# Optimization experiments

Measured on AMD Instinct MI355X. Metric: run time of the kernel, lower is better.

Reference implementation:

```python
import jax, jax.numpy as jnp
import numpy as np

BN_EPS = 1e-5


def _bn(x, gamma, beta, mean, var):
    # inference-form BatchNorm2d over channel dim of NCHW
    inv = gamma / jnp.sqrt(var + BN_EPS)
    return x * inv[None, :, None, None] + (beta - mean * inv)[None, :, None, None]


def _conv(x, w, pad):
    return jax.lax.conv_general_dilated(
        x, w, window_strides=(1, 1), padding=[(pad, pad), (pad, pad)],
        dimension_numbers=("NCHW", "OIHW", "NCHW"))


def setup_inputs() -> dict:
    key = jax.random.key(0)
    ks = jax.random.split(key, 5)
    B, Cin, H, W = 16, 256, 80, 80
    N, Dg, E, Co = 80, 512, 128, 256  # classes, guide dim, embed ch, out ch
    M = 8  # heads
    init = lambda k, shape, fan: jax.random.normal(k, shape, jnp.float32) / np.float32(np.sqrt(fan))
    return {
        "x": jax.random.normal(ks[0], (B, Cin, H, W), jnp.float32),
        "guide": jax.random.normal(ks[1], (B, N, Dg), jnp.float32),
        "embed_w": init(ks[2], (E, Cin, 1, 1), Cin),
        "embed_bn_gamma": jnp.ones((E,), jnp.float32),
        "embed_bn_beta": jnp.zeros((E,), jnp.float32),
        "embed_bn_mean": jnp.zeros((E,), jnp.float32),
        "embed_bn_var": jnp.ones((E,), jnp.float32),
        "guide_w": init(ks[3], (E, Dg), Dg),
        "guide_b": jnp.zeros((E,), jnp.float32),
        "attn_bias": jnp.zeros((M,), jnp.float32),
        "proj_w": init(ks[4], (Co, Cin, 3, 3), Cin * 9),
        "proj_bn_gamma": jnp.ones((Co,), jnp.float32),
        "proj_bn_beta": jnp.zeros((Co,), jnp.float32),
        "proj_bn_mean": jnp.zeros((Co,), jnp.float32),
        "proj_bn_var": jnp.ones((Co,), jnp.float32),
    }


def reference(x, guide, embed_w, embed_bn_gamma, embed_bn_beta, embed_bn_mean,
              embed_bn_var, guide_w, guide_b, attn_bias, proj_w,
              proj_bn_gamma, proj_bn_beta, proj_bn_mean, proj_bn_var):
    B, _, H, W = x.shape
    N = guide.shape[1]
    M = attn_bias.shape[0]
    E = embed_w.shape[0]
    C = E // M  # attn head channels
    # guide projection: [B,N,Dg] -> [B,N,M,C]
    g = (guide @ guide_w.T + guide_b).reshape(B, N, M, C)
    # embed conv (1x1, BN, no act): [B,E,H,W] -> [B,M,C,H,W]
    e = _bn(_conv(x, embed_w, 0), embed_bn_gamma, embed_bn_beta,
            embed_bn_mean, embed_bn_var).reshape(B, M, C, H, W)
    # cross-modal scores, max over classes
    attn = jnp.einsum("bmchw,bnmc->bmhwn", e, g)  # [B,M,H,W,N]
    attn = jnp.max(attn, axis=-1) / float(np.sqrt(C))
    attn = jax.nn.sigmoid(attn + attn_bias[None, :, None, None])  # [B,M,H,W]
    # project conv (3x3, BN, SiLU) and gate per head
    p = jax.nn.silu(_bn(_conv(x, proj_w, 1), proj_bn_gamma, proj_bn_beta,
                        proj_bn_mean, proj_bn_var))
    Co = p.shape[1]
    p = p.reshape(B, M, Co // M, H, W) * attn[:, :, None]
    return p.reshape(B, Co, H, W)
```

## Files before the change

### kernel.cpp

```cpp
#include <hip/hip_runtime.h>
#include <stdint.h>

#define BB 16
#define CIN 256
#define HH 80
#define WW 80
#define HWP (HH*WW)
#define NN 80
#define DG 512
#define EE 128
#define MM 8
#define CC 16
#define CO 256

typedef unsigned short bfu;
typedef _Float16 f16;
typedef _Float16 f16x8 __attribute__((ext_vector_type(8)));
typedef float f32x4 __attribute__((ext_vector_type(4)));

__device__ __forceinline__ float b2f(bfu u) {
    union { uint32_t i; float f; } v; v.i = ((uint32_t)u) << 16; return v.f;
}
__device__ __forceinline__ bfu f2b(float f) {
    union { float f; uint32_t i; } v; v.f = f;
    uint32_t i = v.i;
    return (bfu)((i + 0x7FFFu + ((i >> 16) & 1u)) >> 16);
}
__device__ __forceinline__ float ld(const void* p, size_t i, int f32) {
    if (f32) return ((const float*)p)[i];
    return b2f(((const bfu*)p)[i]);
}
__device__ __forceinline__ int dtf32(const void* dtp) {
    return (((const uint32_t*)dtp)[0] == 0x3F800000u) ? 1 : 0;
}

__device__ __forceinline__ void gld_lds16(const f16* g, f16* l) {
    __builtin_amdgcn_global_load_lds(
        (const __attribute__((address_space(1))) void*)g,
        (__attribute__((address_space(3))) void*)l,
        16, 0, 0);
}

__global__ __launch_bounds__(128) void k_guide(
    const void* __restrict__ guide, const void* __restrict__ guide_w,
    const void* __restrict__ guide_b,
    const void* __restrict__ bng, const void* __restrict__ bnb,
    const void* __restrict__ bnm, const void* __restrict__ bnv,
    float* __restrict__ gs, float* __restrict__ gb)
{
    __shared__ float gld[DG];
    __shared__ float gwL[64][129];
    __shared__ float sh[EE];
    const int f32 = dtf32(bnv);
    const int t = threadIdx.x;
    const int bn = blockIdx.x;
    size_t gbase = (size_t)bn * DG;
    for (int d = t; d < DG; d += 128) gld[d] = ld(guide, gbase + d, f32);
    const int dd = t & 63, eh = t >> 6;
    float acc = 0.f;
    for (int d0 = 0; d0 < DG; d0 += 64) {
        __syncthreads();
        #pragma unroll
        for (int k = 0; k < 64; ++k)
            gwL[dd][eh + 2 * k] = ld(guide_w, (size_t)(eh + 2 * k) * DG + d0 + dd, f32);
        __syncthreads();
        #pragma unroll 8
        for (int d2 = 0; d2 < 64; ++d2)
            acc += gld[d0 + d2] * gwL[d2][t];
    }
    acc += ld(guide_b, t, f32);
    float inv   = ld(bng, t, f32) * rsqrtf(ld(bnv, t, f32) + 1e-5f);
    float shift = ld(bnb, t, f32) - ld(bnm, t, f32) * inv;
    gs[(size_t)bn * EE + t] = acc * inv;
    sh[t] = acc * shift;
    __syncthreads();
    if ((t & 15) == 0) {
        float s = 0.f;
        #pragma unroll
        for (int c = 0; c < 16; ++c) s += sh[t + c];
        gb[bn * MM + (t >> 4)] = s;
    }
}

__global__ __launch_bounds__(256) void k_guidemm(
    const f16* __restrict__ gwH, const f16* __restrict__ guideH,
    const void* __restrict__ guide_b,
    const void* __restrict__ bng, const void* __restrict__ bnb,
    const void* __restrict__ bnm, const void* __restrict__ bnv,
    float* __restrict__ gs, float* __restrict__ gb)
{
    const int f32 = dtf32(bnv);
    const int bn0 = blockIdx.x * 16;
    const int t = threadIdx.x;
    const int w = t >> 6, l = t & 63;
    const int lane15 = l & 15, kg = l >> 4;
    const int e0 = w * 32;

    f32x4 acc0 = {0.f, 0.f, 0.f, 0.f};
    f32x4 acc1 = {0.f, 0.f, 0.f, 0.f};

    const f16* ga  = guideH + (size_t)(bn0 + lane15) * DG + kg * 8;
    const f16* wa0 = gwH + (size_t)(e0 + lane15) * DG + kg * 8;
    const f16* wa1 = gwH + (size_t)(e0 + 16 + lane15) * DG + kg * 8;
    #pragma unroll 4
    for (int d0 = 0; d0 < DG; d0 += 32) {
        f16x8 B  = *(const f16x8*)(ga + d0);
        f16x8 A0 = *(const f16x8*)(wa0 + d0);
        f16x8 A1 = *(const f16x8*)(wa1 + d0);
        acc0 = __builtin_amdgcn_mfma_f32_16x16x32_f16(A0, B, acc0, 0, 0, 0);
        acc1 = __builtin_amdgcn_mfma_f32_16x16x32_f16(A1, B, acc1, 0, 0, 0);
    }
    const int bn = bn0 + lane15;
    float gbp0 = 0.f, gbp1 = 0.f;
    #pragma unroll
    for (int rg = 0; rg < 4; ++rg) {
        {
            int e = e0 + kg * 4 + rg;
            float g = acc0[rg] + ld(guide_b, e, f32);
            float inv   = ld(bng, e, f32) * rsqrtf(ld(bnv, e, f32) + 1e-5f);
            float shift = ld(bnb, e, f32) - ld(bnm, e, f32) * inv;
            gs[(size_t)bn * EE + e] = g * inv;
            gbp0 += g * shift;
        }
        {
            int e = e0 + 16 + kg * 4 + rg;
            float g = acc1[rg] + ld(guide_b, e, f32);
            float inv   = ld(bng, e, f32) * rsqrtf(ld(bnv, e, f32) + 1e-5f);
            float shift = ld(bnb, e, f32) - ld(bnm, e, f32) * inv;
            gs[(size_t)bn * EE + e] = g * inv;
            gbp1 += g * shift;
        }
    }
    gbp0 += __shfl_xor(gbp0, 16);
    gbp0 += __shfl_xor(gbp0, 32);
    gbp1 += __shfl_xor(gbp1, 16);
    gbp1 += __shfl_xor(gbp1, 32);
    if (kg == 0) {
        gb[bn * MM + w * 2 + 0] = gbp0;
        gb[bn * MM + w * 2 + 1] = gbp1;
    }
}

__global__ __launch_bounds__(256) void k_embed(
    const void* __restrict__ x, const void* __restrict__ ew,
    const void* __restrict__ dtp, bfu* __restrict__ eraw)
{
    const int BK = 32;
    __shared__ float Al[32][128];
    __shared__ float Bl[32][128];
    const int f32 = dtf32(dtp);
    int b  = blockIdx.y;
    int p0 = blockIdx.x * 128;
    int t  = threadIdx.x;
    int ty = t >> 4, tx = t & 15;
    float acc[8][8];
    #pragma unroll
    for (int i = 0; i < 8; ++i)
        #pragma unroll
        for (int j = 0; j < 8; ++j) acc[i][j] = 0.f;
    size_t xbase = (size_t)b * CIN * HWP;

    for (int k0 = 0; k0 < CIN; k0 += BK) {
        {
            int e = t >> 1, kh = (t & 1) * 16;
            size_t wb = (size_t)e * CIN + k0 + kh;
            #pragma unroll
            for (int j = 0; j < 16; ++j) Al[kh + j][e] = ld(ew, wb + j, f32);
        }
        {
            int kk = t >> 3, ph = (t & 7) * 16;
            size_t xr = xbase + (size_t)(k0 + kk) * HWP + p0 + ph;
            #pragma unroll
            for (int j = 0; j < 16; ++j) Bl[kk][ph + j] = ld(x, xr + j, f32);
        }
        __syncthreads();
        #pragma unroll
        for (int kk = 0; kk < BK; ++kk) {
            float a[8], bb[8];
            #pragma unroll
            for (int i = 0; i < 8; ++i) a[i]  = Al[kk][ty * 8 + i];
            #pragma unroll
            for (int j = 0; j < 8; ++j) bb[j] = Bl[kk][tx * 8 + j];
            #pragma unroll
            for (int i = 0; i < 8; ++i)
                #pragma unroll
                for (int j = 0; j < 8; ++j) acc[i][j] += a[i] * bb[j];
        }
        __syncthreads();
    }
    #pragma unroll
    for (int i = 0; i < 8; ++i) {
        bfu* orow = eraw + ((size_t)b * EE + ty * 8 + i) * HWP + p0 + tx * 8;
        bfu tmp[8];
        #pragma unroll
        for (int j = 0; j < 8; ++j) tmp[j] = f2b(acc[i][j]);
        #pragma unroll
        for (int j = 0; j < 8; ++j) orow[j] = tmp[j];
    }
}

__global__ __launch_bounds__(256) void k_attn(
    const bfu* __restrict__ eraw, const float* __restrict__ gs,
    const float* __restrict__ gb, const void* __restrict__ attn_bias,
    const void* __restrict__ dtp, float* __restrict__ attn)
{
    __shared__ float gsL[NN * EE];
    __shared__ float gbL[NN * MM];
    const int f32 = dtf32(dtp);
    int b  = blockIdx.y;
    int p0 = blockIdx.x * 128;
    int t  = threadIdx.x;
    const float* gsb = gs + (size_t)b * NN * EE;
    const float* gbb = gb + (size_t)b * NN * MM;
    for (int i = t; i < NN * EE; i += 256) gsL[i] = gsb[i];
    for (int i = t; i < NN * MM; i += 256) gbL[i] = gbb[i];
    __syncthreads();
    int m = t >> 5, pi = t & 31;
    int p = p0 + pi;
    float ev[4][CC];
    #pragma unroll
    for (int c = 0; c < CC; ++c) {
        size_t base = ((size_t)b * EE + m * CC + c) * HWP + p;
        #pragma unroll
        for (int j = 0; j < 4; ++j) ev[j][c] = b2f(eraw[base + j * 32]);
    }
    float mx[4];
    #pragma unroll
    for (int j = 0; j < 4; ++j) mx[j] = -1e30f;
    for (int n = 0; n < NN; ++n) {
        const float* g = gsL + n * EE + m * CC;
        float gv[CC];
        #pragma unroll
        for (int c = 0; c < CC; ++c) gv[c] = g[c];
        float s[4];
        float s0 = gbL[n * MM + m];
        #pragma unroll
        for (int j = 0; j < 4; ++j) s[j] = s0;
        #pragma unroll
        for (int c = 0; c < CC; ++c)
            #pragma unroll
            for (int j = 0; j < 4; ++j) s[j] += gv[c] * ev[j][c];
        #pragma unroll
        for (int j = 0; j < 4; ++j) mx[j] = fmaxf(mx[j], s[j]);
    }
    float bias = ld(attn_bias, m, f32);
    #pragma unroll
    for (int j = 0; j < 4; ++j) {
        float v = mx[j] * 0.25f + bias;
        attn[((size_t)b * MM + m) * HWP + p + j * 32] = 1.f / (1.f + __expf(-v));
    }
}

__global__ __launch_bounds__(256) void k_proj(
    const void* __restrict__ x, const void* __restrict__ pw,
    const void* __restrict__ bng, const void* __restrict__ bnb,
    const void* __restrict__ bnm, const void* __restrict__ bnv,
    const float* __restrict__ attn, void* __restrict__ out)
{
    const int BK = 8;
    __shared__ float Wl[64][73];
    __shared__ float Xl[BK][4][84];
    const int f32 = dtf32(bnv);
    int y0  = blockIdx.x * 2;
    int co0 = blockIdx.y * 64;
    int b   = blockIdx.z;
    int t   = threadIdx.x;
    int tco  = t >> 4;
    int prow = (t & 15) >> 3;
    int pcol = ((t & 15) & 7) * 10;
    float acc[4][10];
    #pragma unroll
    for (int i = 0; i < 4; ++i)
        #pragma unroll
        for (int j = 0; j < 10; ++j) acc[i][j] = 0.f;
    size_t xbase = (size_t)b * CIN * HWP;

    for (int c0 = 0; c0 < CIN; c0 += BK) {
        for (int idx = t; idx < 64 * BK * 9; idx += 256) {
            int co = idx / 72, rem = idx % 72;
            Wl[co][rem] = ld(pw, (size_t)(co0 + co) * 2304 + c0 * 9 + rem, f32);
        }
        for (int idx = t; idx < BK * 4 * 82; idx += 256) {
            int kk = idx / 328, rem = idx % 328;
            int r = rem / 82, cx = rem % 82;
            int y = y0 + r - 1, xc = cx - 1;
            float v = 0.f;
            if (y >= 0 && y < HH && xc >= 0 && xc < WW)
                v = ld(x, xbase + (size_t)(c0 + kk) * HWP + y * WW + xc, f32);
            Xl[kk][r][cx] = v;
        }
        __syncthreads();
        #pragma unroll
        for (int kk = 0; kk < BK; ++kk) {
            #pragma unroll
            for (int ky = 0; ky < 3; ++ky) {
                float xv[12];
                #pragma unroll
                for (int j = 0; j < 12; ++j) xv[j] = Xl[kk][prow + ky][pcol + j];
                float wv[4][3];
                #pragma unroll
                for (int i = 0; i < 4; ++i)
                    #pragma unroll
                    for (int kx = 0; kx < 3; ++kx)
                        wv[i][kx] = Wl[tco * 4 + i][kk * 9 + ky * 3 + kx];
                #pragma unroll
                for (int kx = 0; kx < 3; ++kx)
                    #pragma unroll
                    for (int i = 0; i < 4; ++i)
                        #pragma unroll
                        for (int j = 0; j < 10; ++j)
                            acc[i][j] += wv[i][kx] * xv[j + kx];
            }
        }
        __syncthreads();
    }
    int y = y0 + prow;
    const float* attb = attn + (size_t)b * MM * HWP;
    #pragma unroll
    for (int i = 0; i < 4; ++i) {
        int co = co0 + tco * 4 + i;
        float inv   = ld(bng, co, f32) * rsqrtf(ld(bnv, co, f32) + 1e-5f);
        float shift = ld(bnb, co, f32) - ld(bnm, co, f32) * inv;
        const float* arow = attb + (co >> 5) * HWP + y * WW + pcol;
        size_t obase = ((size_t)b * CO + co) * HWP + (size_t)y * WW + pcol;
        #pragma unroll
        for (int j = 0; j < 10; ++j) {
            float v = acc[i][j] * inv + shift;
            float s = v / (1.f + __expf(-v));
            float r = s * arow[j];
            if (f32) ((float*)out)[obase + j] = r;
            else     ((bfu*)out)[obase + j] = f2b(r);
        }
    }
}


__global__ __launch_bounds__(256) void k_prepx(
    const void* __restrict__ x, const void* __restrict__ dtp,
    f16* __restrict__ xt)
{
    const int f32o = dtf32(dtp);
    const int b  = blockIdx.z;
    const int cg = blockIdx.y;
    const int p  = blockIdx.x * 256 + threadIdx.x;
    if (p >= 82 * 84) return;
    const int ry = p / 84;
    const int cx = p - ry * 84;
    const int y = ry - 1, xx = cx - 1;
    f16* dst = xt + ((size_t)(b * 82 + ry) * 84 + cx) * 256 + cg * 32;
    if (y < 0 || y >= HH || xx < 0 || xx >= WW) {
        uint4 z = make_uint4(0u, 0u, 0u, 0u);
        #pragma unroll
        for (int c = 0; c < 32; c += 8) *(uint4*)(dst + c) = z;
        return;
    }
    const size_t sb = (size_t)b * CIN * HWP + (size_t)(cg * 32) * HWP
                    + (size_t)y * WW + xx;
    #pragma unroll
    for (int c0 = 0; c0 < 32; c0 += 8) {
        f16x8 v;
        #pragma unroll
        for (int j = 0; j < 8; ++j)
            v[j] = (f16)ld(x, sb + (size_t)(c0 + j) * HWP, f32o);
        *(f16x8*)(dst + c0) = v;
    }
}

#define WT_N   (CO * 9 * CIN)
#define WET_N  (EE * CIN)
#define GWH_N  (EE * DG)
#define GDH_N  (BB * NN * DG)
#define PREP_TOT (WT_N + WET_N + GWH_N + GDH_N)
__global__ __launch_bounds__(256) void k_prepw(
    const void* __restrict__ pw, const void* __restrict__ ew,
    const void* __restrict__ gw, const void* __restrict__ gd,
    const void* __restrict__ dtp,
    f16* __restrict__ wt, f16* __restrict__ wet,
    f16* __restrict__ gwH, f16* __restrict__ guideH)
{
    const int f32o = dtf32(dtp);
    const int i = blockIdx.x * 256 + threadIdx.x;
    if (i < WT_N) {
        int ci = i & 255;
        int r9 = i >> 8;
        int tap = r9 % 9, co = r9 / 9;
        wt[i] = (f16)ld(pw, ((size_t)co * CIN + ci) * 9 + tap, f32o);
    } else if (i < WT_N + WET_N) {
        int k = i - WT_N;
        wet[k] = (f16)ld(ew, k, f32o);
    } else if (i < WT_N + WET_N + GWH_N) {
        int k = i - (WT_N + WET_N);
        gwH[k] = (f16)ld(gw, k, f32o);
    } else if (i < PREP_TOT) {
        int k = i - (WT_N + WET_N + GWH_N);
        guideH[k] = (f16)ld(gd, k, f32o);
    }
}

__global__ __launch_bounds__(256, 3) void k_embedmm(
    const f16* __restrict__ xt, const f16* __restrict__ wet,
    bfu* __restrict__ eraw)
{
    __shared__ f16 Xs[2][6144];
    const int n  = blockIdx.x;
    const int L  = (n & 7) * 80 + (n >> 3);
    const int y0 = (L % 40) * 2;
    const int b  = L / 40;
    const int t  = threadIdx.x;
    const int w  = t >> 6, l = t & 63;
    const int lane15 = l & 15, kg = l >> 4;
    const int ew0 = w * 32;

    f32x4 acc[20];
    #pragma unroll
    for (int i = 0; i < 20; ++i) { acc[i][0]=0.f; acc[i][1]=0.f; acc[i][2]=0.f; acc[i][3]=0.f; }

    const size_t xrow = ((size_t)b * 82 + y0 + 1) * 84;
    const f16* wl0 = wet + (size_t)(ew0 + lane15) * 256;
    const f16* wl1 = wet + (size_t)(ew0 + 16 + lane15) * 256;
    const int lbase = (lane15 + 1) * 32 + kg * 8;

    size_t sb0[3];
    #pragma unroll
    for (int k = 0; k < 3; ++k) {
        int c = t + k * 256;
        int cg = c & 3, rcx = c >> 2;
        int r = rcx / 84, cx = rcx - r * 84;
        sb0[k] = ((xrow + (size_t)r * 84 + cx) << 8) + cg * 8;
    }

    #define E_STAGE(buf, c0) { \
        _Pragma("unroll") \
        for (int k = 0; k < 3; ++k) \
            gld_lds16(xt + sb0[k] + (c0), (buf) + w * 512 + k * 2048); }

    f16* rd = &Xs[0][0];
    f16* wr = &Xs[1][0];
    E_STAGE(rd, 0);
    __syncthreads();

    for (int c0 = 0; c0 < 256; c0 += 32) {
        if (c0 < 224) E_STAGE(wr, c0 + 32);
        f16x8 A0 = *(const f16x8*)(wl0 + c0 + kg * 8);
        f16x8 A1 = *(const f16x8*)(wl1 + c0 + kg * 8);
        __builtin_amdgcn_s_setprio(1);
        #pragma unroll
        for (int ct = 0; ct < 5; ++ct) {
            int boff = lbase + ct * 512;
            f16x8 B0 = *(const f16x8*)&rd[boff];
            f16x8 B1 = *(const f16x8*)&rd[boff + 2688];
            acc[ct]      = __builtin_amdgcn_mfma_f32_16x16x32_f16(A0, B0, acc[ct],      0, 0, 0);
            acc[5 + ct]  = __builtin_amdgcn_mfma_f32_16x16x32_f16(A0, B1, acc[5 + ct],  0, 0, 0);
            acc[10 + ct] = __builtin_amdgcn_mfma_f32_16x16x32_f16(A1, B0, acc[10 + ct], 0, 0, 0);
            acc[15 + ct] = __builtin_amdgcn_mfma_f32_16x16x32_f16(A1, B1, acc[15 + ct], 0, 0, 0);
        }
        __builtin_amdgcn_s_setprio(0);
        __syncthreads();
        f16* tmp = rd; rd = wr; wr = tmp;
    }
    const int crow = kg * 4;
    #pragma unroll
    for (int r = 0; r < 2; ++r) {
        int y = y0 + r;
        #pragma unroll
        for (int ct = 0; ct < 5; ++ct)
            #pragma unroll
            for (int d = 0; d < 2; ++d) {
                f32x4 ac = acc[d * 10 + r * 5 + ct];
                #pragma unroll
                for (int rg = 0; rg < 4; ++rg) {
                    int e = ew0 + d * 16 + crow + rg;
                    size_t oi = ((size_t)b * EE + e) * HWP + (size_t)y * WW + ct * 16 + lane15;
                    eraw[oi] = f2b(ac[rg]);
                }
            }
    }
    #undef E_STAGE
}

__global__ __launch_bounds__(256, 3) void k_projmm(
    const f16* __restrict__ xt, const f16* __restrict__ wt,
    const void* __restrict__ bng, const void* __restrict__ bnb,
    const void* __restrict__ bnm, const void* __restrict__ bnv,
    const float* __restrict__ attn, void* __restrict__ out)
{
    __shared__ f16 Xs[2][10752];
    const int f32o = dtf32(bnv);
    const int n   = blockIdx.x;
    const int L   = (n & 7) * 160 + (n >> 3);
    const int co0 = (L & 1) * 128;
    const int y0  = ((L >> 1) % 40) * 2;
    const int b   = L / 80;
    const int t   = threadIdx.x;
    const int w   = t >> 6, l = t & 63;
    const int lane15 = l & 15, kg = l >> 4;
    const int cow = co0 + w * 32;

    f32x4 acc[20];
    #pragma unroll
    for (int i = 0; i < 20; ++i) { acc[i][0]=0.f; acc[i][1]=0.f; acc[i][2]=0.f; acc[i][3]=0.f; }

    const size_t xrow = ((size_t)b * 82 + y0) * 84;
    const f16* wl0 = wt + (size_t)(cow + lane15) * 2304;
    const f16* wl1 = wt + (size_t)(cow + 16 + lane15) * 2304;
    const int lbase = lane15 * 32 + kg * 8;

    size_t sb0[6];
    #pragma unroll
    for (int k = 0; k < 6; ++k) {
        int c = t + k * 256;
        int cg = c & 3, rcx = c >> 2;
        int r = rcx / 84, cx = rcx - r * 84;
        sb0[k] = ((xrow + (size_t)r * 84 + cx) << 8) + cg * 8;
    }

    #define P_STAGE(buf, c0) { \
        _Pragma("unroll") \
        for (int k = 0; k < 5; ++k) \
            gld_lds16(xt + sb0[k] + (c0), (buf) + w * 512 + k * 2048); \
        if (w == 0) gld_lds16(xt + sb0[5] + (c0), (buf) + 5 * 2048); }

    f16* rd = &Xs[0][0];
    f16* wr = &Xs[1][0];
    P_STAGE(rd, 0);
    __syncthreads();

    for (int c0 = 0; c0 < 256; c0 += 32) {
        if (c0 < 224) P_STAGE(wr, c0 + 32);
        f16x8 A[2][9];
        #pragma unroll
        for (int tap = 0; tap < 9; ++tap) {
            A[0][tap] = *(const f16x8*)(wl0 + tap * 256 + c0 + kg * 8);
            A[1][tap] = *(const f16x8*)(wl1 + tap * 256 + c0 + kg * 8);
        }
        __builtin_amdgcn_s_setprio(1);
        #pragma unroll
        for (int ct = 0; ct < 5; ++ct)
            #pragma unroll
            for (int s = 0; s < 3; ++s) {
                int boff = lbase + (ct * 16 + s) * 32;
                f16x8 B0 = *(const f16x8*)&rd[boff];
                f16x8 B1 = *(const f16x8*)&rd[boff + 2688];
                f16x8 B2 = *(const f16x8*)&rd[boff + 5376];
                f16x8 B3 = *(const f16x8*)&rd[boff + 8064];
                #pragma unroll
                for (int ky = 0; ky < 3; ++ky) {
                    f16x8 a0 = A[0][ky * 3 + s];
                    f16x8 a1 = A[1][ky * 3 + s];
                    f16x8 br0 = (ky == 0) ? B0 : (ky == 1) ? B1 : B2;
                    f16x8 br1 = (ky == 0) ? B1 : (ky == 1) ? B2 : B3;
                    acc[ct]      = __builtin_amdgcn_mfma_f32_16x16x32_f16(a0, br0, acc[ct],      0, 0, 0);
                    acc[5 + ct]  = __builtin_amdgcn_mfma_f32_16x16x32_f16(a0, br1, acc[5 + ct],  0, 0, 0);
                    acc[10 + ct] = __builtin_amdgcn_mfma_f32_16x16x32_f16(a1, br0, acc[10 + ct], 0, 0, 0);
                    acc[15 + ct] = __builtin_amdgcn_mfma_f32_16x16x32_f16(a1, br1, acc[15 + ct], 0, 0, 0);
                }
            }
        __builtin_amdgcn_s_setprio(0);
        __syncthreads();
        f16* tmp = rd; rd = wr; wr = tmp;
    }
    const int crow = kg * 4;
    float invv[2][4], shv[2][4];
    #pragma unroll
    for (int d = 0; d < 2; ++d)
        #pragma unroll
        for (int rg = 0; rg < 4; ++rg) {
            int co = cow + d * 16 + crow + rg;
            float iv = ld(bng, co, f32o) * rsqrtf(ld(bnv, co, f32o) + 1e-5f);
            invv[d][rg] = iv;
            shv[d][rg]  = ld(bnb, co, f32o) - ld(bnm, co, f32o) * iv;
        }
    const float* ab = attn + ((size_t)b * MM + (cow >> 5)) * HWP;
    #pragma unroll
    for (int r = 0; r < 2; ++r) {
        int y = y0 + r;
        #pragma unroll
        for (int ct = 0; ct < 5; ++ct) {
            float av = ab[y * WW + ct * 16 + lane15];
            #pragma unroll
            for (int d = 0; d < 2; ++d) {
                f32x4 ac = acc[d * 10 + r * 5 + ct];
                #pragma unroll
                for (int rg = 0; rg < 4; ++rg) {
                    int co = cow + d * 16 + crow + rg;
                    float v = ac[rg] * invv[d][rg] + shv[d][rg];
                    float sv = v / (1.f + __expf(-v));
                    float rv = sv * av;
                    size_t oi = ((size_t)b * CO + co) * HWP + (size_t)y * WW + ct * 16 + lane15;
                    if (f32o) ((float*)out)[oi] = rv;
                    else      ((bfu*)out)[oi]  = f2b(rv);
                }
            }
        }
    }
    #undef P_STAGE
}

extern "C" void kernel_launch(void* const* d_in, const int* in_sizes, int n_in,
                              void* d_out, int out_size, void* d_ws, size_t ws_size,
                              hipStream_t stream) {
    const void* x        = d_in[0];
    const void* guide    = d_in[1];
    const void* embed_w  = d_in[2];
    const void* e_bng    = d_in[3];
    const void* e_bnb    = d_in[4];
    const void* e_bnm    = d_in[5];
    const void* e_bnv    = d_in[6];
    const void* guide_w  = d_in[7];
    const void* guide_b  = d_in[8];
    const void* attn_bias= d_in[9];
    const void* proj_w   = d_in[10];
    const void* p_bng    = d_in[11];
    const void* p_bnb    = d_in[12];
    const void* p_bnm    = d_in[13];
    const void* p_bnv    = d_in[14];

    float* gs   = (float*)((char*)d_ws + 256);
    float* gb   = (float*)((char*)d_ws + 655616);
    bfu*   eraw = (bfu*)((char*)d_ws + 696576);
    float* attn = (float*)((char*)d_ws + 26910976);
    const size_t NEED = 89301248;

    if (ws_size >= NEED) {
        f16* xt     = (f16*)((char*)d_ws + 30187776);
        f16* wt     = (f16*)((char*)d_ws + 86614272);
        f16* wet    = (f16*)((char*)d_ws + 87793920);
        f16* gwH    = (f16*)((char*)d_ws + 87859456);
        f16* guideH = (f16*)((char*)d_ws + 87990528);
        hipLaunchKernelGGL(k_prepw, dim3(PREP_TOT / 256), dim3(256), 0, stream,
                           proj_w, embed_w, guide_w, guide, e_bnv, wt, wet, gwH, guideH);
        hipLaunchKernelGGL(k_guidemm, dim3(BB * NN / 16), dim3(256), 0, stream,
                           gwH, guideH, guide_b, e_bng, e_bnb, e_bnm, e_bnv, gs, gb);
        hipLaunchKernelGGL(k_prepx, dim3(27, 8, BB), dim3(256), 0, stream,
                           x, e_bnv, xt);
        hipLaunchKernelGGL(k_embedmm, dim3(640), dim3(256), 0, stream,
                           xt, wet, eraw);
        hipLaunchKernelGGL(k_attn, dim3(50, BB), dim3(256), 0, stream,
                           eraw, gs, gb, attn_bias, e_bnv, attn);
        hipLaunchKernelGGL(k_projmm, dim3(1280), dim3(256), 0, stream,
                           xt, wt, p_bng, p_bnb, p_bnm, p_bnv, attn, d_out);
    } else {
        hipLaunchKernelGGL(k_guide, dim3(BB * NN), dim3(128), 0, stream,
                           guide, guide_w, guide_b, e_bng, e_bnb, e_bnm, e_bnv, gs, gb);
        hipLaunchKernelGGL(k_embed, dim3(50, BB), dim3(256), 0, stream,
                           x, embed_w, e_bnv, eraw);
        hipLaunchKernelGGL(k_attn, dim3(50, BB), dim3(256), 0, stream,
                           eraw, gs, gb, attn_bias, e_bnv, attn);
        hipLaunchKernelGGL(k_proj, dim3(40, 4, BB), dim3(256), 0, stream,
                           x, proj_w, p_bng, p_bnb, p_bnm, p_bnv, attn, d_out);
    }
}
```

Baseline: 480.1 us.

## Swizzle LDS channel groups to avoid bank conflicts and remap prepx threads

```diff
diff --git a/kernel.cpp b/kernel.cpp
--- a/kernel.cpp
+++ b/kernel.cpp
@@ -340,21 +340,21 @@
     f16* __restrict__ xt)
 {
     const int f32o = dtf32(dtp);
-    const int b  = blockIdx.z;
-    const int cg = blockIdx.y;
-    const int p  = blockIdx.x * 256 + threadIdx.x;
-    if (p >= 82 * 84) return;
-    const int ry = p / 84;
-    const int cx = p - ry * 84;
+    const int b   = blockIdx.y;
+    const int pix = blockIdx.x * 32 + (threadIdx.x >> 3);
+    const int oc  = (threadIdx.x & 7) * 32;
+    if (pix >= 82 * 84) return;
+    const int ry = pix / 84;
+    const int cx = pix - ry * 84;
     const int y = ry - 1, xx = cx - 1;
-    f16* dst = xt + ((size_t)(b * 82 + ry) * 84 + cx) * 256 + cg * 32;
+    f16* dst = xt + ((size_t)(b * 82 + ry) * 84 + cx) * 256 + oc;
     if (y < 0 || y >= HH || xx < 0 || xx >= WW) {
         uint4 z = make_uint4(0u, 0u, 0u, 0u);
         #pragma unroll
         for (int c = 0; c < 32; c += 8) *(uint4*)(dst + c) = z;
         return;
     }
-    const size_t sb = (size_t)b * CIN * HWP + (size_t)(cg * 32) * HWP
+    const size_t sb = (size_t)b * CIN * HWP + (size_t)oc * HWP
                     + (size_t)y * WW + xx;
     #pragma unroll
     for (int c0 = 0; c0 < 32; c0 += 8) {
@@ -418,7 +418,6 @@
     const size_t xrow = ((size_t)b * 82 + y0 + 1) * 84;
     const f16* wl0 = wet + (size_t)(ew0 + lane15) * 256;
     const f16* wl1 = wet + (size_t)(ew0 + 16 + lane15) * 256;
-    const int lbase = (lane15 + 1) * 32 + kg * 8;
 
     size_t sb0[3];
     #pragma unroll
@@ -426,7 +425,8 @@
         int c = t + k * 256;
         int cg = c & 3, rcx = c >> 2;
         int r = rcx / 84, cx = rcx - r * 84;
-        sb0[k] = ((xrow + (size_t)r * 84 + cx) << 8) + cg * 8;
+        sb0[k] = ((xrow + (size_t)r * 84 + cx) << 8)
+               + (size_t)((cg ^ ((cx >> 1) & 3)) * 8);
     }
 
     #define E_STAGE(buf, c0) { \
@@ -446,7 +446,8 @@
         __builtin_amdgcn_s_setprio(1);
         #pragma unroll
         for (int ct = 0; ct < 5; ++ct) {
-            int boff = lbase + ct * 512;
+            int cxv = lane15 + 1 + ct * 16;
+            int boff = cxv * 32 + ((kg ^ ((cxv >> 1) & 3)) << 3);
             f16x8 B0 = *(const f16x8*)&rd[boff];
             f16x8 B1 = *(const f16x8*)&rd[boff + 2688];
             acc[ct]      = __builtin_amdgcn_mfma_f32_16x16x32_f16(A0, B0, acc[ct],      0, 0, 0);
@@ -503,7 +504,6 @@
     const size_t xrow = ((size_t)b * 82 + y0) * 84;
     const f16* wl0 = wt + (size_t)(cow + lane15) * 2304;
     const f16* wl1 = wt + (size_t)(cow + 16 + lane15) * 2304;
-    const int lbase = lane15 * 32 + kg * 8;
 
     size_t sb0[6];
     #pragma unroll
@@ -511,7 +511,8 @@
         int c = t + k * 256;
         int cg = c & 3, rcx = c >> 2;
         int r = rcx / 84, cx = rcx - r * 84;
-        sb0[k] = ((xrow + (size_t)r * 84 + cx) << 8) + cg * 8;
+        sb0[k] = ((xrow + (size_t)r * 84 + cx) << 8)
+               + (size_t)((cg ^ ((cx >> 1) & 3)) * 8);
     }
 
     #define P_STAGE(buf, c0) { \
@@ -538,7 +539,8 @@
         for (int ct = 0; ct < 5; ++ct)
             #pragma unroll
             for (int s = 0; s < 3; ++s) {
-                int boff = lbase + (ct * 16 + s) * 32;
+                int cxv = ct * 16 + s + lane15;
+                int boff = cxv * 32 + ((kg ^ ((cxv >> 1) & 3)) << 3);
                 f16x8 B0 = *(const f16x8*)&rd[boff];
                 f16x8 B1 = *(const f16x8*)&rd[boff + 2688];
                 f16x8 B2 = *(const f16x8*)&rd[boff + 5376];
@@ -631,7 +633,7 @@
                            proj_w, embed_w, guide_w, guide, e_bnv, wt, wet, gwH, guideH);
         hipLaunchKernelGGL(k_guidemm, dim3(BB * NN / 16), dim3(256), 0, stream,
                            gwH, guideH, guide_b, e_bng, e_bnb, e_bnm, e_bnv, gs, gb);
-        hipLaunchKernelGGL(k_prepx, dim3(27, 8, BB), dim3(256), 0, stream,
+        hipLaunchKernelGGL(k_prepx, dim3(216, BB), dim3(256), 0, stream,
                            x, e_bnv, xt);
         hipLaunchKernelGGL(k_embedmm, dim3(640), dim3(256), 0, stream,
                            xt, wet, eraw);
```

After: 554.1 us. +15.4%, slower.
